# Kernel tuning notes

Measured on AMD Instinct MI355X. Metric: run time of the kernel, lower is better.

## Reference

```python
import jax, jax.numpy as jnp
import numpy as np

NUM_EXPERTS = 8
IN_FEATURES = 2048
OUT_FEATURES = 2048
TOTAL_TOKENS = 32768


def setup_inputs() -> dict:
    key = jax.random.key(0)
    k1, k2, k3 = jax.random.split(key, 3)
    input_tokens = jax.random.normal(k1, (TOTAL_TOKENS, IN_FEATURES), dtype=jnp.float32)
    expert_assignments = jax.random.randint(k2, (TOTAL_TOKENS,), 0, NUM_EXPERTS, dtype=jnp.int32)
    # kaiming_uniform_ with a=sqrt(2): bound = sqrt(6 / ((1 + a^2) * fan_in)) = sqrt(2 / fan_in)
    bound = float(np.sqrt(2.0 / IN_FEATURES))
    weight = jax.random.uniform(k3, (NUM_EXPERTS, OUT_FEATURES, IN_FEATURES),
                                dtype=jnp.float32, minval=-bound, maxval=bound)
    return {"input_tokens": input_tokens, "expert_assignments": expert_assignments, "weight": weight}


def reference(input_tokens, expert_assignments, weight):
    # Grouped GEMM: out[t] = input_tokens[t] @ weight[assign[t]].T
    # Each token belongs to exactly one expert, so masked accumulation over the
    # small fixed expert set reproduces the original sort+per-expert-mm+scatter math.
    num_experts = weight.shape[0]
    out = jnp.zeros((input_tokens.shape[0], weight.shape[1]), dtype=input_tokens.dtype)
    for e in range(num_experts):
        mask = (expert_assignments == e)[:, None]  # [T, 1]
        # zero out tokens not owned by this expert before the GEMM so the
        # contribution is exact (matmul of zero rows yields zero rows)
        xe = jnp.where(mask, input_tokens, 0.0)  # [T, in]
        out = out + xe @ weight[e].T  # [T, out]
    return out
```

## Files before the change

kernel.cpp:

```cpp
#include <hip/hip_runtime.h>
#include <hip/hip_bf16.h>

#define NEXP 8
#define KIN 2048
#define NOUT 2048
#define NTOK 32768

#define BM 256
#define BN 256
#define BK 64

#define NBLK (NTOK / 256)
#define MAXTILE (NTOK / BM + NEXP - 1)

typedef unsigned int u32;
typedef unsigned short u16;
typedef __bf16 bf16x8 __attribute__((ext_vector_type(8)));
typedef float f32x4 __attribute__((ext_vector_type(4)));

__device__ __forceinline__ u16 f2bf(float f) {
    u32 u = __float_as_uint(f);
    u += 0x7FFFu + ((u >> 16) & 1u);
    return (u16)(u >> 16);
}

__device__ __forceinline__ void load_lds16(const void* g, void* l) {
    __builtin_amdgcn_global_load_lds(
        (const __attribute__((address_space(1))) u32*)g,
        (__attribute__((address_space(3))) u32*)l, 16, 0, 0);
}

__global__ void rank_k(const int* __restrict__ assign, int* __restrict__ counts,
                       int* __restrict__ rank, int* __restrict__ blockBase) {
    __shared__ int lc[NEXP];
    int t = blockIdx.x * 256 + threadIdx.x;
    if (threadIdx.x < NEXP) lc[threadIdx.x] = 0;
    __syncthreads();
    int e = assign[t];
    rank[t] = atomicAdd(&lc[e], 1);
    __syncthreads();
    if (threadIdx.x < NEXP)
        blockBase[blockIdx.x * NEXP + threadIdx.x] =
            atomicAdd(&counts[threadIdx.x], lc[threadIdx.x]);
}

__global__ void prefix_k(int* __restrict__ ctrl, int4* __restrict__ tileTable) {
    __shared__ int cnt[NEXP], ts[NEXP + 1], tstart[NEXP + 1];
    int t = threadIdx.x;
    if (t < NEXP) cnt[t] = ctrl[t];
    __syncthreads();
    if (t == 0) {
        int s = 0, tile = 0;
        for (int e = 0; e < NEXP; e++) {
            ts[e] = s; tstart[e] = tile;
            s += cnt[e]; tile += (cnt[e] + BM - 1) / BM;
        }
        ts[NEXP] = s; tstart[NEXP] = tile;
        for (int e = 0; e <= NEXP; e++) ctrl[8 + e] = ts[e];
    }
    __syncthreads();
    for (int tt = t; tt < MAXTILE; tt += blockDim.x) {
        int4 v = make_int4(0, 0, 0, 0);
#pragma unroll
        for (int e = 0; e < NEXP; e++) {
            if (tt >= tstart[e] && tt < tstart[e + 1]) {
                int i = tt - tstart[e];
                v = make_int4(ts[e] + i * BM, ts[e] + cnt[e], e, 0);
            }
        }
        tileTable[tt] = v;
    }
}

__global__ void scatter_k(const int* __restrict__ assign, const int* __restrict__ ctrl,
                          const int* __restrict__ rank, const int* __restrict__ blockBase,
                          int* __restrict__ list) {
    __shared__ int base[NEXP];
    int t = blockIdx.x * 256 + threadIdx.x;
    if (threadIdx.x < NEXP)
        base[threadIdx.x] = ctrl[8 + threadIdx.x] +
                            blockBase[blockIdx.x * NEXP + threadIdx.x];
    __syncthreads();
    list[base[assign[t]] + rank[t]] = t;
}

__global__ void conv2_k(const float* __restrict__ A, u16* __restrict__ Ab,
                        const float* __restrict__ W, u16* __restrict__ Wb) {
    const size_t AV = (size_t)NTOK * KIN / 8;
    size_t v = (size_t)blockIdx.x * 256 + threadIdx.x;
    const float* src; u16* dst; size_t i;
    if (v < AV) { src = A; dst = Ab; i = v << 3; }
    else        { src = W; dst = Wb; i = (v - AV) << 3; }
    const float4* s = (const float4*)(src + i);
    float4 f0 = s[0], f1 = s[1];
    uint4 o;
    o.x = (u32)f2bf(f0.x) | ((u32)f2bf(f0.y) << 16);
    o.y = (u32)f2bf(f0.z) | ((u32)f2bf(f0.w) << 16);
    o.z = (u32)f2bf(f1.x) | ((u32)f2bf(f1.y) << 16);
    o.w = (u32)f2bf(f1.z) | ((u32)f2bf(f1.w) << 16);
    *(uint4*)(dst + i) = o;
}

#define BARS() asm volatile("s_barrier" ::: "memory")
#define WVM(N) asm volatile("s_waitcnt vmcnt(" #N ")" ::: "memory")

__global__ __launch_bounds__(512, 2) void gemm_k(const u16* __restrict__ Ab,
                                                 const u16* __restrict__ Wb,
                                                 const int* __restrict__ list,
                                                 const int4* __restrict__ tileTable,
                                                 float* __restrict__ out) {
    extern __shared__ char sh[];
    int* listLds = (int*)(sh + 131072);

    int orig = blockIdx.x;
    int sid = (orig & 7) * (MAXTILE) + (orig >> 3);
    int4 tt = tileTable[sid >> 3];
    int rowBase = tt.x, rowEnd = tt.y, e = tt.z;
    if (rowEnd <= rowBase) return;
    int nBase = (sid & 7) * BN;
    int tid = threadIdx.x;
    int lane = tid & 63, w = tid >> 6;
    int wm = w >> 2, wn = w & 3;

    if (tid < BM) listLds[tid] = list[min(rowBase + tid, rowEnd - 1)];
    __syncthreads();

    int srow = (w << 4) + (lane >> 3);
    u32 ksoB = (u32)((((lane & 7) ^ (lane >> 3)) << 4));
    u32 aO00 = (u32)listLds[srow] * 4096u + ksoB;
    u32 aO01 = (u32)listLds[srow + 8] * 4096u + ksoB;
    u32 aO10 = (u32)listLds[srow + 128] * 4096u + ksoB;
    u32 aO11 = (u32)listLds[srow + 136] * 4096u + ksoB;
    u32 bO0 = (u32)(e * NOUT + nBase + srow) * 4096u + ksoB;
    u32 bO1 = bO0 + 128u * 4096u;
    u32 ldsOff = (u32)((w << 11) + (lane << 4));

#define STA(H, m, b) { char* d_ = sh + (b) * 65536 + (H) * 16384 + ldsOff;          \
        load_lds16((const char*)Ab + aO##H##0 + (m) * 128, d_);                      \
        load_lds16((const char*)Ab + aO##H##1 + (m) * 128, d_ + 1024); }
#define STB(H, m, b) { char* d_ = sh + (b) * 65536 + 32768 + (H) * 16384 + ldsOff;   \
        load_lds16((const char*)Wb + bO##H + (m) * 128, d_);                         \
        load_lds16((const char*)Wb + bO##H + 32768u + (m) * 128, d_ + 1024); }

    u32 s0 = (u32)((((lane >> 4) ^ (lane & 7)) << 4));
    u32 aRow = (u32)((wm * 128 + (lane & 15)) * 128);
    u32 bRow = (u32)(32768 + (wn * 64 + (lane & 15)) * 128);

    bf16x8 ra0[4][2], ra1[4][2], rb0[2][2], rb1[2][2];
    f32x4 acc[8][4];
#pragma unroll
    for (int i = 0; i < 8; ++i)
#pragma unroll
        for (int j = 0; j < 4; ++j) acc[i][j] = (f32x4){0.f, 0.f, 0.f, 0.f};

#define RDA(dst, mf0, b) { _Pragma("unroll") for (int m_ = 0; m_ < 4; ++m_) {        \
        const char* p_ = sh + (b) * 65536 + aRow + ((mf0) + m_) * 2048;              \
        dst[m_][0] = *(const bf16x8*)(p_ + s0);                                      \
        dst[m_][1] = *(const bf16x8*)(p_ + (s0 ^ 64)); } }
#define RDB(dst, nf0, b) { _Pragma("unroll") for (int n_ = 0; n_ < 2; ++n_) {        \
        const char* p_ = sh + (b) * 65536 + bRow + ((nf0) + n_) * 2048;              \
        dst[n_][0] = *(const bf16x8*)(p_ + s0);                                      \
        dst[n_][1] = *(const bf16x8*)(p_ + (s0 ^ 64)); } }

#define QUAD(RA, RB, MO, NO) { __builtin_amdgcn_s_setprio(1);                        \
    _Pragma("unroll") for (int m_ = 0; m_ < 4; ++m_)                                 \
    _Pragma("unroll") for (int n_ = 0; n_ < 2; ++n_) {                               \
        acc[(MO)+m_][(NO)+n_] = __builtin_amdgcn_mfma_f32_16x16x32_bf16(             \
            RA[m_][0], RB[n_][0], acc[(MO)+m_][(NO)+n_], 0, 0, 0);                   \
        acc[(MO)+m_][(NO)+n_] = __builtin_amdgcn_mfma_f32_16x16x32_bf16(             \
            RA[m_][1], RB[n_][1], acc[(MO)+m_][(NO)+n_], 0, 0, 0); }                 \
    __builtin_amdgcn_s_setprio(0); }

    STA(0, 0, 0); STA(1, 0, 0); STB(0, 0, 0); STB(1, 0, 0);
    STB(0, 1, 1); STB(1, 1, 1); STA(0, 1, 1);
    WVM(6);
    BARS();
    RDA(ra0, 0, 0); RDB(rb0, 0, 0);

    for (int j = 0; j < 30; ++j) {
        int b = j & 1, nb = b ^ 1;
        RDB(rb1, 2, b);
        STA(1, j + 1, nb);
        QUAD(ra0, rb0, 0, 0);
        BARS();
        RDA(ra1, 4, b);
        STB(0, j + 2, b);
        QUAD(ra0, rb1, 0, 2);
        BARS();
        STB(1, j + 2, b);
        QUAD(ra1, rb0, 4, 0);
        BARS();
        WVM(4);
        BARS();
        RDA(ra0, 0, nb);
        RDB(rb0, 0, nb);
        STA(0, j + 2, b);
        QUAD(ra1, rb1, 4, 2);
        BARS();
    }

    RDB(rb1, 2, 0);
    STA(1, 31, 1);
    QUAD(ra0, rb0, 0, 0);
    BARS();
    RDA(ra1, 4, 0);
    QUAD(ra0, rb1, 0, 2);
    BARS();
    QUAD(ra1, rb0, 4, 0);
    BARS();
    WVM(0);
    BARS();
    RDA(ra0, 0, 1);
    RDB(rb0, 0, 1);
    QUAD(ra1, rb1, 4, 2);
    RDB(rb1, 2, 1);
    QUAD(ra0, rb0, 0, 0);
    RDA(ra1, 4, 1);
    QUAD(ra0, rb1, 0, 2);
    QUAD(ra1, rb0, 4, 0);
    QUAD(ra1, rb1, 4, 2);

    int cnt = rowEnd - rowBase;
    int cb = nBase + wn * 64 + (lane & 15);
#pragma unroll
    for (int mf = 0; mf < 8; ++mf) {
        int r0 = wm * 128 + mf * 16 + ((lane >> 4) << 2);
#pragma unroll
        for (int rr = 0; rr < 4; ++rr) {
            int rl = r0 + rr;
            if (rl < cnt) {
                float* orow = out + (size_t)listLds[rl] * NOUT + cb;
#pragma unroll
                for (int nf = 0; nf < 4; ++nf) orow[nf * 16] = acc[mf][nf][rr];
            }
        }
    }
#undef STA
#undef STB
#undef RDA
#undef RDB
#undef QUAD
}

__global__ void fallback_k(const float* __restrict__ A, const int* __restrict__ assign,
                           const float* __restrict__ W, float* __restrict__ out) {
    long idx = (long)blockIdx.x * 256 + threadIdx.x;
    int t = (int)(idx >> 11);
    int n = (int)(idx & (NOUT - 1));
    int e = assign[t];
    const float4* a = (const float4*)(A + (size_t)t * KIN);
    const float4* w = (const float4*)(W + ((size_t)e * NOUT + n) * KIN);
    float s = 0.f;
    for (int k = 0; k < KIN / 4; k++) {
        float4 x = a[k], y = w[k];
        s += x.x * y.x + x.y * y.y + x.z * y.z + x.w * y.w;
    }
    out[idx] = s;
}

extern "C" void kernel_launch(void* const* d_in, const int* in_sizes, int n_in,
                              void* d_out, int out_size, void* d_ws, size_t ws_size,
                              hipStream_t stream) {
    const float* A = (const float*)d_in[0];
    const int* assign = (const int*)d_in[1];
    const float* W = (const float*)d_in[2];
    float* out = (float*)d_out;

    const size_t Ab_bytes = (size_t)NTOK * KIN * 2;
    const size_t Wb_bytes = (size_t)NEXP * NOUT * KIN * 2;
    const size_t list_bytes = (size_t)NTOK * 4;
    const size_t rank_bytes = (size_t)NTOK * 4;
    const size_t bb_bytes = (size_t)NBLK * NEXP * 4;
    const size_t ctrl_bytes = 256;
    const size_t tt_bytes = (size_t)MAXTILE * 16;
    const size_t need = Ab_bytes + Wb_bytes + list_bytes + rank_bytes +
                        bb_bytes + ctrl_bytes + tt_bytes;

    if (ws_size < need) {
        fallback_k<<<(NTOK * (long)NOUT) / 256, 256, 0, stream>>>(A, assign, W, out);
        return;
    }

    char* p = (char*)d_ws;
    u16* Ab = (u16*)p;                     p += Ab_bytes;
    u16* Wb = (u16*)p;                     p += Wb_bytes;
    int* list = (int*)p;                   p += list_bytes;
    int* rank = (int*)p;                   p += rank_bytes;
    int* blockBase = (int*)p;              p += bb_bytes;
    int* ctrl = (int*)p;                   p += ctrl_bytes;
    int4* tileTable = (int4*)p;

    static bool attr_done = false;
    if (!attr_done) {
        hipFuncSetAttribute((const void*)gemm_k,
                            hipFuncAttributeMaxDynamicSharedMemorySize, 132096);
        attr_done = true;
    }

    hipMemsetAsync(ctrl, 0, ctrl_bytes, stream);
    rank_k<<<NBLK, 256, 0, stream>>>(assign, ctrl, rank, blockBase);
    prefix_k<<<1, 256, 0, stream>>>(ctrl, tileTable);
    scatter_k<<<NBLK, 256, 0, stream>>>(assign, ctrl, rank, blockBase, list);
    const int conv_blocks = (int)(((size_t)NTOK * KIN / 8 + (size_t)NEXP * NOUT * KIN / 8) / 256);
    conv2_k<<<conv_blocks, 256, 0, stream>>>(A, Ab, W, Wb);
    gemm_k<<<8 * MAXTILE, 512, 132096, stream>>>(Ab, Wb, list, tileTable, out);
}
```

Before: 789.3 us.

## Fuse token gather with bf16 conversion and make grouped GEMM persistent

Replaces the scatter kernel and the combined A/W conversion with a gather kernel that converts activations to bf16 and writes them contiguously in expert-sorted order, plus a separate weight conversion. The GEMM becomes a persistent kernel with one block per slot that pulls tiles from an atomic counter. It prefetches the next tile's first K stages while finishing and storing the current tile. This is meant to remove launch tail effects, indirect row addressing, and pipeline fill bubbles. The cost is extra atomics and barriers per tile, and a tile order that may change W reuse in cache.

```diff
diff --git a/kernel.cpp b/kernel.cpp
--- a/kernel.cpp
+++ b/kernel.cpp
@@ -57,6 +57,8 @@
         }
         ts[NEXP] = s; tstart[NEXP] = tile;
         for (int e = 0; e <= NEXP; e++) ctrl[8 + e] = ts[e];
+        ctrl[18] = tile * 8;
+        ctrl[19] = 256;
     }
     __syncthreads();
     for (int tt = t; tt < MAXTILE; tt += blockDim.x) {
@@ -72,25 +74,33 @@
     }
 }
 
-__global__ void scatter_k(const int* __restrict__ assign, const int* __restrict__ ctrl,
-                          const int* __restrict__ rank, const int* __restrict__ blockBase,
-                          int* __restrict__ list) {
-    __shared__ int base[NEXP];
-    int t = blockIdx.x * 256 + threadIdx.x;
-    if (threadIdx.x < NEXP)
-        base[threadIdx.x] = ctrl[8 + threadIdx.x] +
-                            blockBase[blockIdx.x * NEXP + threadIdx.x];
-    __syncthreads();
-    list[base[assign[t]] + rank[t]] = t;
-}
-
-__global__ void conv2_k(const float* __restrict__ A, u16* __restrict__ Ab,
-                        const float* __restrict__ W, u16* __restrict__ Wb) {
-    const size_t AV = (size_t)NTOK * KIN / 8;
-    size_t v = (size_t)blockIdx.x * 256 + threadIdx.x;
-    const float* src; u16* dst; size_t i;
-    if (v < AV) { src = A; dst = Ab; i = v << 3; }
-    else        { src = W; dst = Wb; i = (v - AV) << 3; }
+__global__ void gather_k(const float* __restrict__ A, const int* __restrict__ assign,
+                         const int* __restrict__ rank, const int* __restrict__ blockBase,
+                         const int* __restrict__ ctrl, u16* __restrict__ Ag,
+                         int* __restrict__ list) {
+    int tid = threadIdx.x;
+    int tok = blockIdx.x * 8 + (tid >> 5);
+    int l = tid & 31;
+    int e = assign[tok];
+    int dst = ctrl[8 + e] + blockBase[(tok >> 8) * NEXP + e] + rank[tok];
+    if (l == 0) list[dst] = tok;
+    const float4* s = (const float4*)(A + (size_t)tok * KIN);
+    uint4* d = (uint4*)(Ag + (size_t)dst * KIN);
+#pragma unroll
+    for (int it = 0; it < 8; ++it) {
+        int q = it * 32 + l;
+        float4 f0 = s[q * 2], f1 = s[q * 2 + 1];
+        uint4 o;
+        o.x = (u32)f2bf(f0.x) | ((u32)f2bf(f0.y) << 16);
+        o.y = (u32)f2bf(f0.z) | ((u32)f2bf(f0.w) << 16);
+        o.z = (u32)f2bf(f1.x) | ((u32)f2bf(f1.y) << 16);
+        o.w = (u32)f2bf(f1.z) | ((u32)f2bf(f1.w) << 16);
+        d[q] = o;
+    }
+}
+
+__global__ void conv_k(const float* __restrict__ src, u16* __restrict__ dst) {
+    size_t i = ((size_t)blockIdx.x * 256 + threadIdx.x) << 3;
     const float4* s = (const float4*)(src + i);
     float4 f0 = s[0], f1 = s[1];
     uint4 o;
@@ -103,55 +113,46 @@
 
 #define BARS() asm volatile("s_barrier" ::: "memory")
 #define WVM(N) asm volatile("s_waitcnt vmcnt(" #N ")" ::: "memory")
+#define WLG0() asm volatile("s_waitcnt lgkmcnt(0)" ::: "memory")
 
 __global__ __launch_bounds__(512, 2) void gemm_k(const u16* __restrict__ Ab,
                                                  const u16* __restrict__ Wb,
                                                  const int* __restrict__ list,
                                                  const int4* __restrict__ tileTable,
+                                                 int* ctrl,
                                                  float* __restrict__ out) {
     extern __shared__ char sh[];
     int* listLds = (int*)(sh + 131072);
-
-    int orig = blockIdx.x;
-    int sid = (orig & 7) * (MAXTILE) + (orig >> 3);
-    int4 tt = tileTable[sid >> 3];
-    int rowBase = tt.x, rowEnd = tt.y, e = tt.z;
-    if (rowEnd <= rowBase) return;
-    int nBase = (sid & 7) * BN;
+    volatile int* shsid = (volatile int*)(sh + 132096);
+
+    int total = ctrl[18];
     int tid = threadIdx.x;
     int lane = tid & 63, w = tid >> 6;
     int wm = w >> 2, wn = w & 3;
 
-    if (tid < BM) listLds[tid] = list[min(rowBase + tid, rowEnd - 1)];
-    __syncthreads();
-
     int srow = (w << 4) + (lane >> 3);
     u32 ksoB = (u32)((((lane & 7) ^ (lane >> 3)) << 4));
-    u32 aO00 = (u32)listLds[srow] * 4096u + ksoB;
-    u32 aO01 = (u32)listLds[srow + 8] * 4096u + ksoB;
-    u32 aO10 = (u32)listLds[srow + 128] * 4096u + ksoB;
-    u32 aO11 = (u32)listLds[srow + 136] * 4096u + ksoB;
-    u32 bO0 = (u32)(e * NOUT + nBase + srow) * 4096u + ksoB;
-    u32 bO1 = bO0 + 128u * 4096u;
     u32 ldsOff = (u32)((w << 11) + (lane << 4));
-
-#define STA(H, m, b) { char* d_ = sh + (b) * 65536 + (H) * 16384 + ldsOff;          \
-        load_lds16((const char*)Ab + aO##H##0 + (m) * 128, d_);                      \
-        load_lds16((const char*)Ab + aO##H##1 + (m) * 128, d_ + 1024); }
-#define STB(H, m, b) { char* d_ = sh + (b) * 65536 + 32768 + (H) * 16384 + ldsOff;   \
-        load_lds16((const char*)Wb + bO##H + (m) * 128, d_);                         \
-        load_lds16((const char*)Wb + bO##H + 32768u + (m) * 128, d_ + 1024); }
-
     u32 s0 = (u32)((((lane >> 4) ^ (lane & 7)) << 4));
     u32 aRow = (u32)((wm * 128 + (lane & 15)) * 128);
     u32 bRow = (u32)(32768 + (wn * 64 + (lane & 15)) * 128);
 
-    bf16x8 ra0[4][2], ra1[4][2], rb0[2][2], rb1[2][2];
-    f32x4 acc[8][4];
-#pragma unroll
-    for (int i = 0; i < 8; ++i)
-#pragma unroll
-        for (int j = 0; j < 4; ++j) acc[i][j] = (f32x4){0.f, 0.f, 0.f, 0.f};
+    int sid = blockIdx.x;
+    if (sid >= total) return;
+    int4 tt = tileTable[sid >> 3];
+    int cnt = tt.y - tt.x;
+    int cb = (sid & 7) * BN + wn * 64 + (lane & 15);
+    u32 aO = (u32)(tt.x + srow) * 4096u + ksoB;
+    u32 bO = (u32)(tt.z * NOUT + (sid & 7) * BN + srow) * 4096u + ksoB;
+    int vvn = 0;
+    if (tid < 256) vvn = list[min(tt.x + tid, NTOK - 1)];
+
+#define STA(o, m, b, H) { char* d_ = sh + (b) * 65536 + (H) * 16384 + ldsOff;        \
+        load_lds16((const char*)Ab + (o) + (H) * 524288u + (m) * 128, d_);            \
+        load_lds16((const char*)Ab + (o) + (H) * 524288u + (m) * 128 + 32768u, d_ + 1024); }
+#define STB(o, m, b, H) { char* d_ = sh + (b) * 65536 + 32768 + (H) * 16384 + ldsOff; \
+        load_lds16((const char*)Wb + (o) + (H) * 524288u + (m) * 128, d_);            \
+        load_lds16((const char*)Wb + (o) + (H) * 524288u + (m) * 128 + 32768u, d_ + 1024); }
 
 #define RDA(dst, mf0, b) { _Pragma("unroll") for (int m_ = 0; m_ < 4; ++m_) {        \
         const char* p_ = sh + (b) * 65536 + aRow + ((mf0) + m_) * 2048;              \
@@ -171,69 +172,103 @@
             RA[m_][1], RB[n_][1], acc[(MO)+m_][(NO)+n_], 0, 0, 0); }                 \
     __builtin_amdgcn_s_setprio(0); }
 
-    STA(0, 0, 0); STA(1, 0, 0); STB(0, 0, 0); STB(1, 0, 0);
-    STB(0, 1, 1); STB(1, 1, 1); STA(0, 1, 1);
-    WVM(6);
-    BARS();
-    RDA(ra0, 0, 0); RDB(rb0, 0, 0);
-
-    for (int j = 0; j < 30; ++j) {
-        int b = j & 1, nb = b ^ 1;
-        RDB(rb1, 2, b);
-        STA(1, j + 1, nb);
+    bf16x8 ra0[4][2], ra1[4][2], rb0[2][2], rb1[2][2];
+    f32x4 acc[8][4];
+
+    STA(aO, 0, 0, 0); STA(aO, 0, 0, 1); STB(bO, 0, 0, 0); STB(bO, 0, 0, 1);
+    STB(bO, 1, 1, 0); STB(bO, 1, 1, 1); STA(aO, 1, 1, 0);
+
+    for (;;) {
+        WVM(0);
+        BARS();
+        if (tid < 256) listLds[tid] = vvn;
+        RDA(ra0, 0, 0); RDB(rb0, 0, 0);
+#pragma unroll
+        for (int i = 0; i < 8; ++i)
+#pragma unroll
+            for (int j = 0; j < 4; ++j) acc[i][j] = (f32x4){0.f, 0.f, 0.f, 0.f};
+
+        for (int j = 0; j < 30; ++j) {
+            int b = j & 1, nb = b ^ 1;
+            RDB(rb1, 2, b);
+            STA(aO, j + 1, nb, 1);
+            QUAD(ra0, rb0, 0, 0);
+            BARS();
+            RDA(ra1, 4, b);
+            STB(bO, j + 2, b, 0);
+            QUAD(ra0, rb1, 0, 2);
+            BARS();
+            STB(bO, j + 2, b, 1);
+            QUAD(ra1, rb0, 4, 0);
+            BARS();
+            WVM(4);
+            BARS();
+            RDA(ra0, 0, nb);
+            RDB(rb0, 0, nb);
+            STA(aO, j + 2, b, 0);
+            QUAD(ra1, rb1, 4, 2);
+            BARS();
+        }
+
+        RDB(rb1, 2, 0);
+        STA(aO, 31, 1, 1);
         QUAD(ra0, rb0, 0, 0);
         BARS();
-        RDA(ra1, 4, b);
-        STB(0, j + 2, b);
+        RDA(ra1, 4, 0);
         QUAD(ra0, rb1, 0, 2);
         BARS();
-        STB(1, j + 2, b);
         QUAD(ra1, rb0, 4, 0);
         BARS();
-        WVM(4);
-        BARS();
-        RDA(ra0, 0, nb);
-        RDB(rb0, 0, nb);
-        STA(0, j + 2, b);
+        WVM(0);
+        BARS();
+
+        if (tid == 0) *shsid = atomicAdd(&ctrl[19], 1);
+        WLG0();
+        BARS();
+        int sid2 = *shsid;
+        int have2 = sid2 < total;
+        int cnt2 = 0, cb2 = 0, vvn2 = 0;
+        u32 aO2 = 0, bO2 = 0;
+        if (have2) {
+            int4 t2 = tileTable[sid2 >> 3];
+            cnt2 = t2.y - t2.x;
+            cb2 = (sid2 & 7) * BN + wn * 64 + (lane & 15);
+            aO2 = (u32)(t2.x + srow) * 4096u + ksoB;
+            bO2 = (u32)(t2.z * NOUT + (sid2 & 7) * BN + srow) * 4096u + ksoB;
+            if (tid < 256) vvn2 = list[min(t2.x + tid, NTOK - 1)];
+        }
+
+        RDA(ra0, 0, 1); RDB(rb0, 0, 1);
         QUAD(ra1, rb1, 4, 2);
-        BARS();
-    }
-
-    RDB(rb1, 2, 0);
-    STA(1, 31, 1);
-    QUAD(ra0, rb0, 0, 0);
-    BARS();
-    RDA(ra1, 4, 0);
-    QUAD(ra0, rb1, 0, 2);
-    BARS();
-    QUAD(ra1, rb0, 4, 0);
-    BARS();
-    WVM(0);
-    BARS();
-    RDA(ra0, 0, 1);
-    RDB(rb0, 0, 1);
-    QUAD(ra1, rb1, 4, 2);
-    RDB(rb1, 2, 1);
-    QUAD(ra0, rb0, 0, 0);
-    RDA(ra1, 4, 1);
-    QUAD(ra0, rb1, 0, 2);
-    QUAD(ra1, rb0, 4, 0);
-    QUAD(ra1, rb1, 4, 2);
-
-    int cnt = rowEnd - rowBase;
-    int cb = nBase + wn * 64 + (lane & 15);
-#pragma unroll
-    for (int mf = 0; mf < 8; ++mf) {
-        int r0 = wm * 128 + mf * 16 + ((lane >> 4) << 2);
-#pragma unroll
-        for (int rr = 0; rr < 4; ++rr) {
-            int rl = r0 + rr;
-            if (rl < cnt) {
-                float* orow = out + (size_t)listLds[rl] * NOUT + cb;
-#pragma unroll
-                for (int nf = 0; nf < 4; ++nf) orow[nf * 16] = acc[mf][nf][rr];
+        if (have2) {
+            STA(aO2, 0, 0, 0); STA(aO2, 0, 0, 1);
+            STB(bO2, 0, 0, 0); STB(bO2, 0, 0, 1);
+        }
+        RDB(rb1, 2, 1);
+        QUAD(ra0, rb0, 0, 0);
+        RDA(ra1, 4, 1);
+        QUAD(ra0, rb1, 0, 2);
+        QUAD(ra1, rb0, 4, 0);
+        QUAD(ra1, rb1, 4, 2);
+
+#pragma unroll
+        for (int mf = 0; mf < 8; ++mf) {
+            int r0 = wm * 128 + mf * 16 + ((lane >> 4) << 2);
+#pragma unroll
+            for (int rr = 0; rr < 4; ++rr) {
+                int rl = r0 + rr;
+                if (rl < cnt) {
+                    float* orow = out + (size_t)listLds[rl] * NOUT + cb;
+#pragma unroll
+                    for (int nf = 0; nf < 4; ++nf) orow[nf * 16] = acc[mf][nf][rr];
+                }
             }
         }
+        if (!have2) return;
+
+        STB(bO2, 1, 1, 0); STB(bO2, 1, 1, 1); STA(aO2, 1, 1, 0);
+
+        cnt = cnt2; cb = cb2; aO = aO2; bO = bO2; vvn = vvn2;
     }
 #undef STA
 #undef STB
@@ -293,15 +328,14 @@
     static bool attr_done = false;
     if (!attr_done) {
         hipFuncSetAttribute((const void*)gemm_k,
-                            hipFuncAttributeMaxDynamicSharedMemorySize, 132096);
+                            hipFuncAttributeMaxDynamicSharedMemorySize, 132352);
         attr_done = true;
     }
 
     hipMemsetAsync(ctrl, 0, ctrl_bytes, stream);
     rank_k<<<NBLK, 256, 0, stream>>>(assign, ctrl, rank, blockBase);
     prefix_k<<<1, 256, 0, stream>>>(ctrl, tileTable);
-    scatter_k<<<NBLK, 256, 0, stream>>>(assign, ctrl, rank, blockBase, list);
-    const int conv_blocks = (int)(((size_t)NTOK * KIN / 8 + (size_t)NEXP * NOUT * KIN / 8) / 256);
-    conv2_k<<<conv_blocks, 256, 0, stream>>>(A, Ab, W, Wb);
-    gemm_k<<<8 * MAXTILE, 512, 132096, stream>>>(Ab, Wb, list, tileTable, out);
-}
+    gather_k<<<NTOK / 8, 256, 0, stream>>>(A, assign, rank, blockBase, ctrl, Ab, list);
+    conv_k<<<(NEXP * NOUT * (KIN / 8)) / 256, 256, 0, stream>>>(W, Wb);
+    gemm_k<<<256, 512, 132352, stream>>>(Ab, Wb, list, tileTable, ctrl, out);
+}
```

Result: slower. 882.5 us (+11.8%).
